# Optimization experiments

Measured on AMD Instinct MI355X. Metric: run time of the kernel, lower is better.

Reference implementation:

```python
import jax, jax.numpy as jnp
import numpy as np

NEG_SLOPE = 0.2
EPS = 1e-16


def gat_layer(x, src, dst, W, att, bias, heads, out_ch, concat, num_nodes, edge_weight):
    """WeightedGATConv forward (eval mode, dropout off).
    x: [N, Fin], src/dst: [E], W: [Fin, H*C], att: [H, 2C], bias: [H*C] or [C].
    """
    H, C = heads, out_ch
    xp = (x @ W).reshape(-1, H, C)           # [N, H, C]
    xi = xp[dst]                              # target features  [E, H, C]
    xj = xp[src]                              # source features  [E, H, C]
    # attention logits: (cat(xi, xj) * att).sum(-1)
    alpha = jnp.einsum('ehc,hc->eh', xi, att[:, :C]) + jnp.einsum('ehc,hc->eh', xj, att[:, C:])
    alpha = jnp.where(alpha >= 0, alpha, NEG_SLOPE * alpha)   # leaky_relu
    # segment softmax over incoming edges of each destination node
    amax = jax.ops.segment_max(alpha, dst, num_segments=num_nodes)  # [N, H]
    amax = jnp.where(jnp.isfinite(amax), amax, 0.0)
    ex = jnp.exp(alpha - amax[dst])                                  # [E, H]
    denom = jax.ops.segment_sum(ex, dst, num_segments=num_nodes)     # [N, H]
    a = ex / (denom[dst] + EPS)                                      # [E, H]
    msg = xj * a[..., None]                                          # [E, H, C]
    if edge_weight is not None:
        msg = msg * edge_weight[:, None, None]
    out = jax.ops.segment_sum(msg, dst, num_segments=num_nodes)      # [N, H, C]
    out = out.reshape(num_nodes, H * C) if concat else out.mean(axis=1)
    return out + bias


def setup_inputs() -> dict:
    key = jax.random.key(0)
    ks = jax.random.split(key, 10)
    N, E = 20000, 320000
    IN, HID, LAT, H = 512, 256, 128, 4
    C1 = HID // H
    glorot = lambda k, shp: jax.random.uniform(k, shp, jnp.float32, -1.0, 1.0) * jnp.sqrt(6.0 / (shp[-2] + shp[-1]))
    return {
        'x': jax.random.normal(ks[0], (N, IN), jnp.float32),
        'edge_index': jax.random.randint(ks[1], (2, E), 0, N, jnp.int32),
        'edge_weight': jax.random.uniform(ks[2], (E,), jnp.float32),
        'W1': glorot(ks[3], (IN, H * C1)),
        'att1': glorot(ks[4], (H, 2 * C1)),
        'b1': jnp.zeros((H * C1,), jnp.float32),
        'Wmu': glorot(ks[5], (HID, LAT)),
        'attmu': glorot(ks[6], (1, 2 * LAT)),
        'bmu': jnp.zeros((LAT,), jnp.float32),
        'Wlv': glorot(ks[7], (HID, LAT)),
        'attlv': glorot(ks[8], (1, 2 * LAT)),
        'blv': jnp.zeros((LAT,), jnp.float32),
    }


def reference(x, edge_index, edge_weight, W1, att1, b1, Wmu, attmu, bmu, Wlv, attlv, blv):
    N = x.shape[0]
    src, dst = edge_index[0], edge_index[1]
    H = att1.shape[0]
    C1 = att1.shape[1] // 2
    LAT = Wmu.shape[1]
    h = gat_layer(x, src, dst, W1, att1, b1, H, C1, True, N, edge_weight)
    h = jax.nn.elu(h)
    mu = gat_layer(h, src, dst, Wmu, attmu, bmu, 1, LAT, False, N, edge_weight)
    logvar = gat_layer(h, src, dst, Wlv, attlv, blv, 1, LAT, False, N, edge_weight)
    return (mu, logvar)
```

## Files before the change

kernel.cpp:

```cpp
#include <hip/hip_runtime.h>
#include <stdint.h>

#define NEG_SLOPE 0.2f
#define SEPS 1e-16f

typedef short bf16x8 __attribute__((ext_vector_type(8)));
typedef float f32x4 __attribute__((ext_vector_type(4)));

static __device__ __forceinline__ float bf2f(ushort u) {
  union { uint32_t i; float f; } v; v.i = ((uint32_t)u) << 16; return v.f;
}
static __device__ __forceinline__ ushort f2bf(float f) {
  uint32_t b = __float_as_uint(f);
  b += 0x7FFFu + ((b >> 16) & 1u);
  return (ushort)(b >> 16);
}
static __device__ __forceinline__ float blo(uint32_t u) { return __uint_as_float(u << 16); }
static __device__ __forceinline__ float bhi(uint32_t u) { return __uint_as_float(u & 0xFFFF0000u); }
static __device__ __forceinline__ float ldf(const void* p, size_t i, int mode) {
  return mode ? ((const float*)p)[i] : bf2f(((const ushort*)p)[i]);
}

__global__ void fill_out(float* __restrict__ out, int n, float v) {
  int i = blockIdx.x * 256 + threadIdx.x;
  if (i < n) out[i] = v;
}

struct DetPtrs {
  const uint32_t* p[11];
  int n[11];
  const uint32_t* idx;
  int idxn;
};
__global__ void prologue(DetPtrs dp, int* __restrict__ modes,
                         int* __restrict__ deg, float* __restrict__ dots,
                         int N, int nbDeg) {
  int b = blockIdx.x;
  if (b >= 12) {
    int rb = b - 12;
    if (rb < nbDeg) {
      int i = rb * 256 + threadIdx.x;
      if (i < N) deg[i] = 0;
    } else {
      int i = (rb - nbDeg) * 256 + threadIdx.x;
      if (i < N * 12) dots[i] = 0.f;
    }
    return;
  }
  __shared__ int sL, sH;
  if (threadIdx.x == 0) { sL = 0; sH = 0; }
  __syncthreads();
  if (b < 11) {
    const uint32_t* w = dp.p[b];
    int elems = dp.n[b];
    int nprobe = min(2048, elems / 2);
    int cL = 0, cH = 0;
    for (int i = threadIdx.x; i < nprobe; i += 256) {
      uint32_t v = w[i];
      uint32_t eL = (v >> 7) & 0xFFu;
      uint32_t eH = (v >> 23) & 0xFFu;
      if (eL >= 90u && eL <= 128u) cL++;
      if (eH >= 90u && eH <= 128u) cH++;
    }
    atomicAdd(&sL, cL); atomicAdd(&sH, cH);
    __syncthreads();
    if (threadIdx.x == 0) {
      int m;
      if (sL * 4 >= nprobe * 3) m = 0;
      else if (sH * 4 >= nprobe) m = 1;
      else m = 0;
      modes[b] = m;
    }
  } else {
    const uint32_t* w = dp.idx;
    int nprobe = min(4096, dp.idxn);
    int c = 0;
    for (int i = threadIdx.x; i < nprobe; i += 256)
      if ((i & 1) && w[i] == 0u) c++;
    atomicAdd(&sL, c);
    __syncthreads();
    if (threadIdx.x == 0) modes[11] = (sL * 4 >= (nprobe / 2) * 3) ? 1 : 0;
  }
}

struct WTArgs {
  const void* w1; const void* wmu; const void* wlv;
  ushort* wt1; ushort* wall;
};
struct SmallCan { const void* src[6]; float* dst[6]; int n[6]; int mi[6]; };
struct CanArgs {
  const void* ei; const void* ew;
  int* srcc; int* dstc; int* deg; float* ewf;
  int E; int N; int EB1; int WB;
  WTArgs wt;
  SmallCan sc;
};
__global__ void canon_all(CanArgs a, const int* __restrict__ modes) {
  int b = blockIdx.x;
  if (b < a.EB1) {
    int i = b * 256 + threadIdx.x;
    if (i >= a.E) return;
    int s, d;
    if (modes[11]) {
      s = (int)((const long long*)a.ei)[i];
      d = (int)((const long long*)a.ei)[a.E + i];
    } else {
      s = ((const int*)a.ei)[i];
      d = ((const int*)a.ei)[a.E + i];
    }
    s = min(max(s, 0), a.N - 1);
    d = min(max(d, 0), a.N - 1);
    a.srcc[i] = s;
    a.dstc[i] = d;
    atomicAdd(&a.deg[d], 1);
    float v = ldf(a.ew, i, modes[1]);
    if (!isfinite(v)) v = 0.f;
    a.ewf[i] = v;
  } else if (b < a.EB1 + a.WB) {
    int i = (b - a.EB1) * 256 + threadIdx.x;
    const int NW1 = 256 * 512;
    if (i < NW1) {
      int n = i >> 9, k = i & 511;
      float v = ldf(a.wt.w1, (size_t)k * 256 + n, modes[2]);
      if (!isfinite(v)) v = 0.f;
      a.wt.wt1[i] = f2bf(v);
    } else {
      int j = i - NW1;
      if (j >= 256 * 256) return;
      int n = j >> 8, k = j & 255;
      float v;
      if (n < 128) v = ldf(a.wt.wmu, (size_t)k * 128 + n, modes[5]);
      else         v = ldf(a.wt.wlv, (size_t)k * 128 + (n - 128), modes[8]);
      if (!isfinite(v)) v = 0.f;
      a.wt.wall[j] = f2bf(v);
    }
  } else {
    int sb = b - a.EB1 - a.WB;
    int m = modes[a.sc.mi[sb]];
    const void* s = a.sc.src[sb];
    float* d = a.sc.dst[sb];
    for (int i = threadIdx.x; i < a.sc.n[sb]; i += 256) {
      float v = ldf(s, i, m);
      if (!isfinite(v)) v = 0.f;
      d[i] = v;
    }
  }
}

__global__ __launch_bounds__(1024) void scan_deg(const int* __restrict__ deg,
                                                 int* __restrict__ row_ptr,
                                                 int* __restrict__ row_cur, int N) {
  __shared__ int part[1024];
  int t = threadIdx.x;
  int chunk = (N + 1023) / 1024;
  int lo = t * chunk, hi = min(lo + chunk, N);
  int s = 0;
  for (int i = lo; i < hi; ++i) s += deg[i];
  part[t] = s;
  __syncthreads();
  for (int off = 1; off < 1024; off <<= 1) {
    int v = (t >= off) ? part[t - off] : 0;
    __syncthreads();
    part[t] += v;
    __syncthreads();
  }
  int base = (t == 0) ? 0 : part[t - 1];
  for (int i = lo; i < hi; ++i) {
    row_ptr[i] = base; row_cur[i] = base;
    base += deg[i];
  }
  if (t == 1023) row_ptr[N] = part[1023];
}
__global__ void scatter_edges(const int* __restrict__ dstv, const int* __restrict__ srcv,
                              const float* __restrict__ ew, int* __restrict__ row_cur,
                              int* __restrict__ csr_src, float* __restrict__ csr_w, int E) {
  int e = blockIdx.x * 256 + threadIdx.x;
  if (e < E) {
    int p = atomicAdd(&row_cur[dstv[e]], 1);
    csr_src[p] = srcv[e];
    csr_w[p] = ew[e];
  }
}

template <int KTOT, int DMODE>
__global__ __launch_bounds__(256) void gemm_mfma(
    const void* __restrict__ A, const ushort* __restrict__ WT,
    ushort* __restrict__ out, int M, int nTot,
    const int* __restrict__ modeA, const float* __restrict__ attv,
    float* __restrict__ dotd, float* __restrict__ dotsrc) {
  __shared__ ushort As[64][40];
  __shared__ ushort Bs[128][40];

  int t = threadIdx.x;
  int m0 = blockIdx.x * 64;
  int n0 = blockIdx.y * 128;
  int wid = t >> 6, l = t & 63;
  int wr = wid >> 1, wc = wid & 1;
  int mode = modeA ? *modeA : 1;

  int arow = t >> 2;
  int akoff = (t & 3) * 8;
  int srow = min(m0 + arow, M - 1);
  int brow = t >> 1;
  int bkoff = (t & 1) * 16;

  f32x4 acc[2][4];
#pragma unroll
  for (int i = 0; i < 2; ++i)
#pragma unroll
    for (int j = 0; j < 4; ++j) acc[i][j] = (f32x4){0.f, 0.f, 0.f, 0.f};

  int cl = l & 15;
  int ksl = (l >> 4) * 8;

  for (int k0 = 0; k0 < KTOT; k0 += 32) {
    if (mode) {
      const float* Af = (const float*)A + (size_t)srow * KTOT + k0 + akoff;
      float4 v0 = *(const float4*)Af;
      float4 v1 = *(const float4*)(Af + 4);
      uint4 pk;
      pk.x = (uint32_t)f2bf(v0.x) | ((uint32_t)f2bf(v0.y) << 16);
      pk.y = (uint32_t)f2bf(v0.z) | ((uint32_t)f2bf(v0.w) << 16);
      pk.z = (uint32_t)f2bf(v1.x) | ((uint32_t)f2bf(v1.y) << 16);
      pk.w = (uint32_t)f2bf(v1.z) | ((uint32_t)f2bf(v1.w) << 16);
      *(uint4*)&As[arow][akoff] = pk;
    } else {
      *(uint4*)&As[arow][akoff] =
          *(const uint4*)((const ushort*)A + (size_t)srow * KTOT + k0 + akoff);
    }
    {
      const ushort* wp = WT + (size_t)(n0 + brow) * KTOT + k0 + bkoff;
      *(uint4*)&Bs[brow][bkoff] = *(const uint4*)wp;
      *(uint4*)&Bs[brow][bkoff + 8] = *(const uint4*)(wp + 8);
    }
    __syncthreads();

    bf16x8 af[2], bfr[4];
#pragma unroll
    for (int i = 0; i < 2; ++i)
      af[i] = *(const bf16x8*)&As[wr * 32 + i * 16 + cl][ksl];
#pragma unroll
    for (int j = 0; j < 4; ++j)
      bfr[j] = *(const bf16x8*)&Bs[wc * 64 + j * 16 + cl][ksl];
#pragma unroll
    for (int i = 0; i < 2; ++i)
#pragma unroll
      for (int j = 0; j < 4; ++j)
        acc[i][j] = __builtin_amdgcn_mfma_f32_16x16x32_bf16(af[i], bfr[j], acc[i][j], 0, 0, 0);
    __syncthreads();
  }

  int rb = (l >> 4) * 4;

  if (DMODE) {
    float wd[4], ws[4];
    int hsl;
    if (DMODE == 1) {
      hsl = (n0 >> 6) + wc;
#pragma unroll
      for (int j = 0; j < 4; ++j) {
        wd[j] = attv[hsl * 128 + j * 16 + cl];
        ws[j] = attv[hsl * 128 + 64 + j * 16 + cl];
      }
    } else {
      int base = n0 + wc * 64;
      hsl = base >> 7;
      int ccb = base & 127;
#pragma unroll
      for (int j = 0; j < 4; ++j) {
        wd[j] = attv[hsl * 256 + ccb + j * 16 + cl];
        ws[j] = attv[hsl * 256 + 128 + ccb + j * 16 + cl];
      }
    }
#pragma unroll
    for (int i = 0; i < 2; ++i)
#pragma unroll
      for (int r = 0; r < 4; ++r) {
        float pd = acc[i][0][r] * wd[0] + acc[i][1][r] * wd[1]
                 + acc[i][2][r] * wd[2] + acc[i][3][r] * wd[3];
        float ps = acc[i][0][r] * ws[0] + acc[i][1][r] * ws[1]
                 + acc[i][2][r] * ws[2] + acc[i][3][r] * ws[3];
        pd += __shfl_xor(pd, 1); pd += __shfl_xor(pd, 2);
        pd += __shfl_xor(pd, 4); pd += __shfl_xor(pd, 8);
        ps += __shfl_xor(ps, 1); ps += __shfl_xor(ps, 2);
        ps += __shfl_xor(ps, 4); ps += __shfl_xor(ps, 8);
        if (cl == 0) {
          int m = m0 + wr * 32 + i * 16 + rb + r;
          if (m < M) {
            if (DMODE == 1) {
              atomicAdd(&dotd[m * 4 + hsl], pd);
              atomicAdd(&dotsrc[m * 4 + hsl], ps);
            } else {
              atomicAdd(&dotd[m * 4 + hsl * 2], pd);
              atomicAdd(&dotd[m * 4 + hsl * 2 + 1], ps);
            }
          }
        }
      }
  }

#pragma unroll
  for (int i = 0; i < 2; ++i)
#pragma unroll
    for (int j = 0; j < 4; ++j)
#pragma unroll
      for (int r = 0; r < 4; ++r) {
        int m = m0 + wr * 32 + i * 16 + rb + r;
        if (m < M)
          out[(size_t)m * nTot + n0 + wc * 64 + j * 16 + cl] = f2bf(acc[i][j][r]);
      }
}

__global__ __launch_bounds__(256) void fused_agg1_wave(
    const int* __restrict__ row_ptr, const int* __restrict__ csr_src,
    const float* __restrict__ csr_w,
    const float* __restrict__ ad, const float* __restrict__ as_,
    const ushort* __restrict__ xp, const float* __restrict__ b1,
    float* __restrict__ hout, int N) {
  int n = blockIdx.x * 4 + (threadIdx.x >> 6);
  if (n >= N) return;
  int lane = threadIdx.x & 63;
  int h = lane & 3;
  int es = lane >> 2;
  int sg = lane >> 5, l = lane & 31, hl = l >> 3;

  int lo = row_ptr[n], hi = row_ptr[n + 1];
  float adv = ad[n * 4 + h];

  float m = -1e30f;
  float dsum = 0.f;
  float acc[8];
#pragma unroll
  for (int j = 0; j < 8; ++j) acc[j] = 0.f;

  for (int cb = lo; cb < hi; cb += 16) {
    int cn = min(16, hi - cb);
    float a = -1e30f;
    int sreg = 0;
    float wreg = 0.f;
    if (es < cn) {
      int i = cb + es;
      int s = csr_src[i];
      sreg = s;
      wreg = csr_w[i];
      float aa = adv + as_[s * 4 + h];
      a = aa >= 0.f ? aa : NEG_SLOPE * aa;
    }
    float cm = a;
    cm = fmaxf(cm, __shfl_xor(cm, 4));
    cm = fmaxf(cm, __shfl_xor(cm, 8));
    cm = fmaxf(cm, __shfl_xor(cm, 16));
    cm = fmaxf(cm, __shfl_xor(cm, 32));
    float mnew = fmaxf(m, cm);
    float scale = expf(m - mnew);
    m = mnew;
    float ev = (es < cn) ? expf(a - m) : 0.f;
    dsum = dsum * scale + ev;
    float cwreg = ev * wreg;
    float sc = __shfl(scale, hl);
#pragma unroll
    for (int j = 0; j < 8; ++j) acc[j] *= sc;
    for (int el2 = 0; el2 < cn; el2 += 2) {
      int el = el2 + sg;
      int elc = min(el, cn - 1);
      float cw = __shfl(cwreg, (elc << 2) | hl);
      int s = __shfl(sreg, elc << 2);
      if (el < cn) {
        uint4 v = *(const uint4*)(xp + (size_t)s * 256 + l * 8);
        acc[0] += cw * blo(v.x); acc[1] += cw * bhi(v.x);
        acc[2] += cw * blo(v.y); acc[3] += cw * bhi(v.y);
        acc[4] += cw * blo(v.z); acc[5] += cw * bhi(v.z);
        acc[6] += cw * blo(v.w); acc[7] += cw * bhi(v.w);
      }
    }
  }

  dsum += __shfl_xor(dsum, 4);
  dsum += __shfl_xor(dsum, 8);
  dsum += __shfl_xor(dsum, 16);
  dsum += __shfl_xor(dsum, 32);
  float den = __shfl(dsum, hl);

#pragma unroll
  for (int j = 0; j < 8; ++j) acc[j] += __shfl_down(acc[j], 32);

  if (sg == 0) {
    float inv = 1.0f / (den + SEPS);
#pragma unroll
    for (int j = 0; j < 8; ++j) {
      float val = acc[j] * inv + b1[l * 8 + j];
      hout[(size_t)n * 256 + l * 8 + j] = val > 0.f ? val : expm1f(val);
    }
  }
}

__global__ __launch_bounds__(256) void fused_agg2_wave(
    const int* __restrict__ row_ptr, const int* __restrict__ csr_src,
    const float* __restrict__ csr_w, const float* __restrict__ a4,
    const ushort* __restrict__ hp2,
    const float* __restrict__ bmu, const float* __restrict__ blv,
    float* __restrict__ out, int N) {
  int wid = blockIdx.x * 4 + (threadIdx.x >> 6);
  int n = wid >> 1, sl = wid & 1;
  if (n >= N) return;
  int lane = threadIdx.x & 63;
  int sg = lane >> 4, l = lane & 15;

  int lo = row_ptr[n], hi = row_ptr[n + 1];
  float adv = a4[n * 4 + sl * 2];

  float m = -1e30f;
  float dsum = 0.f;
  float acc[8];
#pragma unroll
  for (int j = 0; j < 8; ++j) acc[j] = 0.f;

  for (int cb = lo; cb < hi; cb += 64) {
    int cn = min(64, hi - cb);
    float a = -1e30f;
    int sreg = 0;
    float wreg = 0.f;
    if (lane < cn) {
      int i = cb + lane;
      int s = csr_src[i];
      sreg = s;
      wreg = csr_w[i];
      float aa = adv + a4[s * 4 + sl * 2 + 1];
      a = aa >= 0.f ? aa : NEG_SLOPE * aa;
    }
    float cm = a;
    cm = fmaxf(cm, __shfl_xor(cm, 1));
    cm = fmaxf(cm, __shfl_xor(cm, 2));
    cm = fmaxf(cm, __shfl_xor(cm, 4));
    cm = fmaxf(cm, __shfl_xor(cm, 8));
    cm = fmaxf(cm, __shfl_xor(cm, 16));
    cm = fmaxf(cm, __shfl_xor(cm, 32));
    float mnew = fmaxf(m, cm);
    float scale = expf(m - mnew);
    m = mnew;
    float ev = (lane < cn) ? expf(a - m) : 0.f;
    dsum = dsum * scale + ev;
    float cwreg = ev * wreg;
#pragma unroll
    for (int j = 0; j < 8; ++j) acc[j] *= scale;
    for (int el2 = 0; el2 < cn; el2 += 4) {
      int el = el2 + sg;
      int elc = min(el, cn - 1);
      float cw = __shfl(cwreg, elc);
      int s = __shfl(sreg, elc);
      if (el < cn) {
        uint4 v = *(const uint4*)(hp2 + (size_t)s * 256 + sl * 128 + l * 8);
        acc[0] += cw * blo(v.x); acc[1] += cw * bhi(v.x);
        acc[2] += cw * blo(v.y); acc[3] += cw * bhi(v.y);
        acc[4] += cw * blo(v.z); acc[5] += cw * bhi(v.z);
        acc[6] += cw * blo(v.w); acc[7] += cw * bhi(v.w);
      }
    }
  }

  dsum += __shfl_xor(dsum, 1);
  dsum += __shfl_xor(dsum, 2);
  dsum += __shfl_xor(dsum, 4);
  dsum += __shfl_xor(dsum, 8);
  dsum += __shfl_xor(dsum, 16);
  dsum += __shfl_xor(dsum, 32);

#pragma unroll
  for (int j = 0; j < 8; ++j) {
    acc[j] += __shfl_down(acc[j], 32);
    acc[j] += __shfl_down(acc[j], 16);
  }

  if (sg == 0) {
    float inv = 1.0f / (dsum + SEPS);
    const float* bb = sl ? blv : bmu;
    float* op = out + (size_t)sl * N * 128 + (size_t)n * 128 + l * 8;
#pragma unroll
    for (int j = 0; j < 8; ++j) op[j] = acc[j] * inv + bb[l * 8 + j];
  }
}

extern "C" void kernel_launch(void* const* d_in, const int* in_sizes, int n_in,
                              void* d_out, int out_size, void* d_ws, size_t ws_size,
                              hipStream_t stream) {
  int OB = (out_size + 255) / 256;
  bool ok = (n_in == 12);
  int HID = 0, IN = 0, N = 0, LAT = 0, E = 0;
  if (ok) {
    HID = in_sizes[5];
    ok = ok && HID == 256;
    IN = HID ? in_sizes[3] / HID : 0;
    ok = ok && IN == 512 && in_sizes[3] == IN * HID;
    N = IN ? in_sizes[0] / IN : 0;
    ok = ok && N > 0 && in_sizes[0] == N * IN && (N % 4) == 0;
    LAT = in_sizes[8];
    ok = ok && LAT == 128;
    E = in_sizes[2];
    ok = ok && E > 0 && in_sizes[1] == 2 * E;
    ok = ok && in_sizes[4] == 2 * HID && in_sizes[6] == HID * LAT &&
         in_sizes[7] == 2 * LAT && in_sizes[9] == HID * LAT &&
         in_sizes[10] == 2 * LAT && in_sizes[11] == LAT &&
         out_size == 2 * N * LAT;
  }
  if (!ok) { fill_out<<<OB, 256, 0, stream>>>((float*)d_out, out_size, 2.0f); return; }

  char* p = (char*)d_ws;
  auto alloc = [&](size_t bytes) -> char* {
    char* r = p;
    p += (bytes + 255) & ~((size_t)255);
    return r;
  };
  ushort* xp_bf = (ushort*)alloc((size_t)N * HID * 2);
  float*  hreg  = (float*) alloc((size_t)N * HID * 4);
  ushort* WT1b  = (ushort*)alloc((size_t)HID * IN * 2);
  ushort* WallT = (ushort*)alloc((size_t)2 * LAT * HID * 2);
  float*  dots  = (float*) alloc((size_t)N * 12 * 4);
  float*  att1f = (float*) alloc((size_t)2 * HID * 4);
  float*  att2f = (float*) alloc((size_t)4 * LAT * 4);
  float*  b1f   = (float*) alloc((size_t)HID * 4);
  float*  bmuf  = (float*) alloc((size_t)LAT * 4);
  float*  blvf  = (float*) alloc((size_t)LAT * 4);
  float*  ewf   = (float*) alloc((size_t)E * 4);
  int*    srcc  = (int*)   alloc((size_t)E * 4);
  int*    dstc  = (int*)   alloc((size_t)E * 4);
  int*    csr_src=(int*)   alloc((size_t)E * 4);
  float*  csr_w = (float*) alloc((size_t)E * 4);
  int*    row_ptr=(int*)   alloc((size_t)(N + 1) * 4);
  int*    row_cur=(int*)   alloc((size_t)N * 4);
  int*    deg   = (int*)   alloc((size_t)N * 4);
  int*    modes = (int*)   alloc(16 * 4);

  size_t need = (size_t)(p - (char*)d_ws);
  if (need > ws_size) {
    fill_out<<<OB, 256, 0, stream>>>((float*)d_out, out_size, 3.0f);
    return;
  }

  ushort* hp2 = xp_bf;
  float* ad1 = dots;
  float* as1 = dots + (size_t)N * 4;
  float* a4  = dots + (size_t)N * 8;

  const int fidx[11] = {0, 2, 3, 4, 5, 6, 7, 8, 9, 10, 11};
  DetPtrs dp;
  for (int i = 0; i < 11; ++i) {
    dp.p[i] = (const uint32_t*)d_in[fidx[i]];
    dp.n[i] = in_sizes[fidx[i]];
  }
  dp.idx = (const uint32_t*)d_in[1];
  dp.idxn = 2 * E;
  int nbDeg = (N + 255) / 256;
  int nbDots = (N * 12 + 255) / 256;
  prologue<<<12 + nbDeg + nbDots, 256, 0, stream>>>(dp, modes, deg, dots, N, nbDeg);

  int EB1 = (E + 255) / 256;
  int WB = (HID * IN + 2 * LAT * HID + 255) / 256;
  CanArgs ca;
  ca.ei = d_in[1]; ca.ew = d_in[2];
  ca.srcc = srcc; ca.dstc = dstc; ca.deg = deg; ca.ewf = ewf;
  ca.E = E; ca.N = N; ca.EB1 = EB1; ca.WB = WB;
  ca.wt.w1 = d_in[3]; ca.wt.wmu = d_in[6]; ca.wt.wlv = d_in[9];
  ca.wt.wt1 = WT1b; ca.wt.wall = WallT;
  ca.sc.src[0] = d_in[4];  ca.sc.dst[0] = att1f;        ca.sc.n[0] = 2 * HID; ca.sc.mi[0] = 3;
  ca.sc.src[1] = d_in[5];  ca.sc.dst[1] = b1f;          ca.sc.n[1] = HID;     ca.sc.mi[1] = 4;
  ca.sc.src[2] = d_in[7];  ca.sc.dst[2] = att2f;        ca.sc.n[2] = 2 * LAT; ca.sc.mi[2] = 6;
  ca.sc.src[3] = d_in[8];  ca.sc.dst[3] = bmuf;         ca.sc.n[3] = LAT;     ca.sc.mi[3] = 7;
  ca.sc.src[4] = d_in[10]; ca.sc.dst[4] = att2f + 256;  ca.sc.n[4] = 2 * LAT; ca.sc.mi[4] = 9;
  ca.sc.src[5] = d_in[11]; ca.sc.dst[5] = blvf;         ca.sc.n[5] = LAT;     ca.sc.mi[5] = 10;
  canon_all<<<EB1 + WB + 6, 256, 0, stream>>>(ca, modes);

  scan_deg<<<1, 1024, 0, stream>>>(deg, row_ptr, row_cur, N);
  scatter_edges<<<EB1, 256, 0, stream>>>(dstc, srcc, ewf, row_cur, csr_src, csr_w, E);

  dim3 g1((N + 63) / 64, HID / 128);
  dim3 g2((N + 63) / 64, (2 * LAT) / 128);

  gemm_mfma<512, 1><<<g1, 256, 0, stream>>>(d_in[0], WT1b, xp_bf, N, HID,
                                            &modes[0], att1f, ad1, as1);
  fused_agg1_wave<<<(N + 3) / 4, 256, 0, stream>>>(row_ptr, csr_src, csr_w,
                                                   ad1, as1, xp_bf, b1f, hreg, N);

  gemm_mfma<256, 2><<<g2, 256, 0, stream>>>(hreg, WallT, hp2, N, 2 * LAT,
                                            nullptr, att2f, a4, nullptr);
  fused_agg2_wave<<<(2 * N + 3) / 4, 256, 0, stream>>>(row_ptr, csr_src, csr_w, a4,
                                                       hp2, bmuf, blvf,
                                                       (float*)d_out, N);
}
```

Measured before the change: 292.0 us.

## Widen GEMM tiles to full N, store bf16 hidden, merge agg2 waves per node

The GEMM now computes all 256 output columns per block, so each A tile is loaded once. Because every attention dot product is complete within one block, the atomics into zeroed buffers become plain stores and the prologue no longer clears the dots array. The first aggregation writes the ELU output as bf16 instead of fp32, which halves that tensor's traffic and lets the second GEMM read bf16 directly. The mu/logvar aggregation now uses one wave per node covering both heads rather than two waves, sharing the edge index loads. The risks are more registers per GEMM thread (16 accumulators), fewer GEMM blocks, and an extra bf16 rounding on the hidden features.

```diff
diff --git a/kernel.cpp b/kernel.cpp
--- a/kernel.cpp
+++ b/kernel.cpp
@@ -33,18 +33,11 @@
   int idxn;
 };
 __global__ void prologue(DetPtrs dp, int* __restrict__ modes,
-                         int* __restrict__ deg, float* __restrict__ dots,
-                         int N, int nbDeg) {
+                         int* __restrict__ deg, int N) {
   int b = blockIdx.x;
   if (b >= 12) {
-    int rb = b - 12;
-    if (rb < nbDeg) {
-      int i = rb * 256 + threadIdx.x;
-      if (i < N) deg[i] = 0;
-    } else {
-      int i = (rb - nbDeg) * 256 + threadIdx.x;
-      if (i < N * 12) dots[i] = 0.f;
-    }
+    int i = (b - 12) * 256 + threadIdx.x;
+    if (i < N) deg[i] = 0;
     return;
   }
   __shared__ int sL, sH;
@@ -185,30 +178,27 @@
 template <int KTOT, int DMODE>
 __global__ __launch_bounds__(256) void gemm_mfma(
     const void* __restrict__ A, const ushort* __restrict__ WT,
-    ushort* __restrict__ out, int M, int nTot,
+    ushort* __restrict__ out, int M,
     const int* __restrict__ modeA, const float* __restrict__ attv,
     float* __restrict__ dotd, float* __restrict__ dotsrc) {
   __shared__ ushort As[64][40];
-  __shared__ ushort Bs[128][40];
+  __shared__ ushort Bs[256][40];
 
   int t = threadIdx.x;
   int m0 = blockIdx.x * 64;
-  int n0 = blockIdx.y * 128;
   int wid = t >> 6, l = t & 63;
   int wr = wid >> 1, wc = wid & 1;
-  int mode = modeA ? *modeA : 1;
+  int mode = modeA ? *modeA : 0;
 
   int arow = t >> 2;
   int akoff = (t & 3) * 8;
   int srow = min(m0 + arow, M - 1);
-  int brow = t >> 1;
-  int bkoff = (t & 1) * 16;
-
-  f32x4 acc[2][4];
+
+  f32x4 acc[2][8];
 #pragma unroll
   for (int i = 0; i < 2; ++i)
 #pragma unroll
-    for (int j = 0; j < 4; ++j) acc[i][j] = (f32x4){0.f, 0.f, 0.f, 0.f};
+    for (int j = 0; j < 8; ++j) acc[i][j] = (f32x4){0.f, 0.f, 0.f, 0.f};
 
   int cl = l & 15;
   int ksl = (l >> 4) * 8;
@@ -228,86 +218,108 @@
       *(uint4*)&As[arow][akoff] =
           *(const uint4*)((const ushort*)A + (size_t)srow * KTOT + k0 + akoff);
     }
-    {
-      const ushort* wp = WT + (size_t)(n0 + brow) * KTOT + k0 + bkoff;
-      *(uint4*)&Bs[brow][bkoff] = *(const uint4*)wp;
-      *(uint4*)&Bs[brow][bkoff + 8] = *(const uint4*)(wp + 8);
+#pragma unroll
+    for (int i = 0; i < 4; ++i) {
+      int f = t + i * 256;
+      int row = f >> 2, koff = (f & 3) * 8;
+      *(uint4*)&Bs[row][koff] = *(const uint4*)(WT + (size_t)row * KTOT + k0 + koff);
     }
     __syncthreads();
 
-    bf16x8 af[2], bfr[4];
+    bf16x8 af[2], bfr[8];
 #pragma unroll
     for (int i = 0; i < 2; ++i)
       af[i] = *(const bf16x8*)&As[wr * 32 + i * 16 + cl][ksl];
 #pragma unroll
-    for (int j = 0; j < 4; ++j)
-      bfr[j] = *(const bf16x8*)&Bs[wc * 64 + j * 16 + cl][ksl];
+    for (int j = 0; j < 8; ++j)
+      bfr[j] = *(const bf16x8*)&Bs[wc * 128 + j * 16 + cl][ksl];
 #pragma unroll
     for (int i = 0; i < 2; ++i)
 #pragma unroll
-      for (int j = 0; j < 4; ++j)
+      for (int j = 0; j < 8; ++j)
         acc[i][j] = __builtin_amdgcn_mfma_f32_16x16x32_bf16(af[i], bfr[j], acc[i][j], 0, 0, 0);
     __syncthreads();
   }
 
   int rb = (l >> 4) * 4;
 
-  if (DMODE) {
-    float wd[4], ws[4];
-    int hsl;
-    if (DMODE == 1) {
-      hsl = (n0 >> 6) + wc;
-#pragma unroll
-      for (int j = 0; j < 4; ++j) {
-        wd[j] = attv[hsl * 128 + j * 16 + cl];
-        ws[j] = attv[hsl * 128 + 64 + j * 16 + cl];
-      }
-    } else {
-      int base = n0 + wc * 64;
-      hsl = base >> 7;
-      int ccb = base & 127;
-#pragma unroll
-      for (int j = 0; j < 4; ++j) {
-        wd[j] = attv[hsl * 256 + ccb + j * 16 + cl];
-        ws[j] = attv[hsl * 256 + 128 + ccb + j * 16 + cl];
-      }
+  if (DMODE == 1) {
+    float wdv[8], wsv[8];
+#pragma unroll
+    for (int j = 0; j < 8; ++j) {
+      int h = wc * 2 + (j >> 2);
+      int c = (j & 3) * 16 + cl;
+      wdv[j] = attv[h * 128 + c];
+      wsv[j] = attv[h * 128 + 64 + c];
     }
 #pragma unroll
     for (int i = 0; i < 2; ++i)
 #pragma unroll
       for (int r = 0; r < 4; ++r) {
-        float pd = acc[i][0][r] * wd[0] + acc[i][1][r] * wd[1]
-                 + acc[i][2][r] * wd[2] + acc[i][3][r] * wd[3];
-        float ps = acc[i][0][r] * ws[0] + acc[i][1][r] * ws[1]
-                 + acc[i][2][r] * ws[2] + acc[i][3][r] * ws[3];
-        pd += __shfl_xor(pd, 1); pd += __shfl_xor(pd, 2);
-        pd += __shfl_xor(pd, 4); pd += __shfl_xor(pd, 8);
-        ps += __shfl_xor(ps, 1); ps += __shfl_xor(ps, 2);
-        ps += __shfl_xor(ps, 4); ps += __shfl_xor(ps, 8);
+        float pd0 = acc[i][0][r] * wdv[0] + acc[i][1][r] * wdv[1]
+                  + acc[i][2][r] * wdv[2] + acc[i][3][r] * wdv[3];
+        float ps0 = acc[i][0][r] * wsv[0] + acc[i][1][r] * wsv[1]
+                  + acc[i][2][r] * wsv[2] + acc[i][3][r] * wsv[3];
+        float pd1 = acc[i][4][r] * wdv[4] + acc[i][5][r] * wdv[5]
+                  + acc[i][6][r] * wdv[6] + acc[i][7][r] * wdv[7];
+        float ps1 = acc[i][4][r] * wsv[4] + acc[i][5][r] * wsv[5]
+                  + acc[i][6][r] * wsv[6] + acc[i][7][r] * wsv[7];
+#pragma unroll
+        for (int d = 1; d < 16; d <<= 1) {
+          pd0 += __shfl_xor(pd0, d); ps0 += __shfl_xor(ps0, d);
+          pd1 += __shfl_xor(pd1, d); ps1 += __shfl_xor(ps1, d);
+        }
         if (cl == 0) {
           int m = m0 + wr * 32 + i * 16 + rb + r;
           if (m < M) {
-            if (DMODE == 1) {
-              atomicAdd(&dotd[m * 4 + hsl], pd);
-              atomicAdd(&dotsrc[m * 4 + hsl], ps);
-            } else {
-              atomicAdd(&dotd[m * 4 + hsl * 2], pd);
-              atomicAdd(&dotd[m * 4 + hsl * 2 + 1], ps);
-            }
+            dotd[m * 4 + wc * 2] = pd0;
+            dotsrc[m * 4 + wc * 2] = ps0;
+            dotd[m * 4 + wc * 2 + 1] = pd1;
+            dotsrc[m * 4 + wc * 2 + 1] = ps1;
           }
         }
       }
+  } else if (DMODE == 2) {
+    float wdv[8], wsv[8];
+#pragma unroll
+    for (int j = 0; j < 8; ++j) {
+      int c = j * 16 + cl;
+      wdv[j] = attv[wc * 256 + c];
+      wsv[j] = attv[wc * 256 + 128 + c];
+    }
+#pragma unroll
+    for (int i = 0; i < 2; ++i)
+#pragma unroll
+      for (int r = 0; r < 4; ++r) {
+        float pd = 0.f, ps = 0.f;
+#pragma unroll
+        for (int j = 0; j < 8; ++j) {
+          pd += acc[i][j][r] * wdv[j];
+          ps += acc[i][j][r] * wsv[j];
+        }
+#pragma unroll
+        for (int d = 1; d < 16; d <<= 1) {
+          pd += __shfl_xor(pd, d); ps += __shfl_xor(ps, d);
+        }
+        if (cl == 0) {
+          int m = m0 + wr * 32 + i * 16 + rb + r;
+          if (m < M) {
+            dotd[m * 4 + wc * 2] = pd;
+            dotd[m * 4 + wc * 2 + 1] = ps;
+          }
+        }
+      }
   }
 
 #pragma unroll
   for (int i = 0; i < 2; ++i)
 #pragma unroll
-    for (int j = 0; j < 4; ++j)
+    for (int j = 0; j < 8; ++j)
 #pragma unroll
       for (int r = 0; r < 4; ++r) {
         int m = m0 + wr * 32 + i * 16 + rb + r;
         if (m < M)
-          out[(size_t)m * nTot + n0 + wc * 64 + j * 16 + cl] = f2bf(acc[i][j][r]);
+          out[(size_t)m * 256 + wc * 128 + j * 16 + cl] = f2bf(acc[i][j][r]);
       }
 }
 
@@ -316,7 +328,7 @@
     const float* __restrict__ csr_w,
     const float* __restrict__ ad, const float* __restrict__ as_,
     const ushort* __restrict__ xp, const float* __restrict__ b1,
-    float* __restrict__ hout, int N) {
+    ushort* __restrict__ hout, int N) {
   int n = blockIdx.x * 4 + (threadIdx.x >> 6);
   if (n >= N) return;
   int lane = threadIdx.x & 63;
@@ -386,11 +398,18 @@
 
   if (sg == 0) {
     float inv = 1.0f / (den + SEPS);
-#pragma unroll
-    for (int j = 0; j < 8; ++j) {
-      float val = acc[j] * inv + b1[l * 8 + j];
-      hout[(size_t)n * 256 + l * 8 + j] = val > 0.f ? val : expm1f(val);
-    }
+    uint4 pk;
+    uint32_t w[4];
+#pragma unroll
+    for (int q = 0; q < 4; ++q) {
+      float v0 = acc[q * 2] * inv + b1[l * 8 + q * 2];
+      float v1 = acc[q * 2 + 1] * inv + b1[l * 8 + q * 2 + 1];
+      v0 = v0 > 0.f ? v0 : expm1f(v0);
+      v1 = v1 > 0.f ? v1 : expm1f(v1);
+      w[q] = (uint32_t)f2bf(v0) | ((uint32_t)f2bf(v1) << 16);
+    }
+    pk.x = w[0]; pk.y = w[1]; pk.z = w[2]; pk.w = w[3];
+    *(uint4*)(hout + (size_t)n * 256 + l * 8) = pk;
   }
 }
 
@@ -400,28 +419,27 @@
     const ushort* __restrict__ hp2,
     const float* __restrict__ bmu, const float* __restrict__ blv,
     float* __restrict__ out, int N) {
-  int wid = blockIdx.x * 4 + (threadIdx.x >> 6);
-  int n = wid >> 1, sl = wid & 1;
+  int n = blockIdx.x * 4 + (threadIdx.x >> 6);
   if (n >= N) return;
   int lane = threadIdx.x & 63;
-  int sg = lane >> 4, l = lane & 15;
+  int e31 = lane & 31, sl = lane >> 5;
 
   int lo = row_ptr[n], hi = row_ptr[n + 1];
   float adv = a4[n * 4 + sl * 2];
 
   float m = -1e30f;
   float dsum = 0.f;
-  float acc[8];
-#pragma unroll
-  for (int j = 0; j < 8; ++j) acc[j] = 0.f;
-
-  for (int cb = lo; cb < hi; cb += 64) {
-    int cn = min(64, hi - cb);
+  float acc[4];
+#pragma unroll
+  for (int j = 0; j < 4; ++j) acc[j] = 0.f;
+
+  for (int cb = lo; cb < hi; cb += 32) {
+    int cn = min(32, hi - cb);
     float a = -1e30f;
     int sreg = 0;
     float wreg = 0.f;
-    if (lane < cn) {
-      int i = cb + lane;
+    if (e31 < cn) {
+      int i = cb + e31;
       int s = csr_src[i];
       sreg = s;
       wreg = csr_w[i];
@@ -434,27 +452,20 @@
     cm = fmaxf(cm, __shfl_xor(cm, 4));
     cm = fmaxf(cm, __shfl_xor(cm, 8));
     cm = fmaxf(cm, __shfl_xor(cm, 16));
-    cm = fmaxf(cm, __shfl_xor(cm, 32));
     float mnew = fmaxf(m, cm);
     float scale = expf(m - mnew);
     m = mnew;
-    float ev = (lane < cn) ? expf(a - m) : 0.f;
+    float ev = (e31 < cn) ? expf(a - m) : 0.f;
     dsum = dsum * scale + ev;
     float cwreg = ev * wreg;
 #pragma unroll
-    for (int j = 0; j < 8; ++j) acc[j] *= scale;
-    for (int el2 = 0; el2 < cn; el2 += 4) {
-      int el = el2 + sg;
-      int elc = min(el, cn - 1);
-      float cw = __shfl(cwreg, elc);
-      int s = __shfl(sreg, elc);
-      if (el < cn) {
-        uint4 v = *(const uint4*)(hp2 + (size_t)s * 256 + sl * 128 + l * 8);
-        acc[0] += cw * blo(v.x); acc[1] += cw * bhi(v.x);
-        acc[2] += cw * blo(v.y); acc[3] += cw * bhi(v.y);
-        acc[4] += cw * blo(v.z); acc[5] += cw * bhi(v.z);
-        acc[6] += cw * blo(v.w); acc[7] += cw * bhi(v.w);
-      }
+    for (int j = 0; j < 4; ++j) acc[j] *= scale;
+    for (int el = 0; el < cn; ++el) {
+      float cw = __shfl(cwreg, (sl << 5) | el);
+      int s = __shfl(sreg, el);
+      uint2 v = *(const uint2*)(hp2 + (size_t)s * 256 + lane * 4);
+      acc[0] += cw * blo(v.x); acc[1] += cw * bhi(v.x);
+      acc[2] += cw * blo(v.y); acc[3] += cw * bhi(v.y);
     }
   }
 
@@ -463,21 +474,13 @@
   dsum += __shfl_xor(dsum, 4);
   dsum += __shfl_xor(dsum, 8);
   dsum += __shfl_xor(dsum, 16);
-  dsum += __shfl_xor(dsum, 32);
-
-#pragma unroll
-  for (int j = 0; j < 8; ++j) {
-    acc[j] += __shfl_down(acc[j], 32);
-    acc[j] += __shfl_down(acc[j], 16);
-  }
-
-  if (sg == 0) {
-    float inv = 1.0f / (dsum + SEPS);
-    const float* bb = sl ? blv : bmu;
-    float* op = out + (size_t)sl * N * 128 + (size_t)n * 128 + l * 8;
-#pragma unroll
-    for (int j = 0; j < 8; ++j) op[j] = acc[j] * inv + bb[l * 8 + j];
-  }
+
+  float inv = 1.0f / (dsum + SEPS);
+  const float* bb = sl ? blv : bmu;
+  int c0 = e31 * 4;
+  float* op = out + (size_t)sl * N * 128 + (size_t)n * 128 + c0;
+#pragma unroll
+  for (int j = 0; j < 4; ++j) op[j] = acc[j] * inv + bb[c0 + j];
 }
 
 extern "C" void kernel_launch(void* const* d_in, const int* in_sizes, int n_in,
@@ -511,7 +514,7 @@
     return r;
   };
   ushort* xp_bf = (ushort*)alloc((size_t)N * HID * 2);
-  float*  hreg  = (float*) alloc((size_t)N * HID * 4);
+  ushort* hreg  = (ushort*)alloc((size_t)N * HID * 2);
   ushort* WT1b  = (ushort*)alloc((size_t)HID * IN * 2);
   ushort* WallT = (ushort*)alloc((size_t)2 * LAT * HID * 2);
   float*  dots  = (float*) alloc((size_t)N * 12 * 4);
@@ -550,8 +553,7 @@
   dp.idx = (const uint32_t*)d_in[1];
   dp.idxn = 2 * E;
   int nbDeg = (N + 255) / 256;
-  int nbDots = (N * 12 + 255) / 256;
-  prologue<<<12 + nbDeg + nbDots, 256, 0, stream>>>(dp, modes, deg, dots, N, nbDeg);
+  prologue<<<12 + nbDeg, 256, 0, stream>>>(dp, modes, deg, N);
 
   int EB1 = (E + 255) / 256;
   int WB = (HID * IN + 2 * LAT * HID + 255) / 256;
@@ -572,17 +574,16 @@
   scan_deg<<<1, 1024, 0, stream>>>(deg, row_ptr, row_cur, N);
   scatter_edges<<<EB1, 256, 0, stream>>>(dstc, srcc, ewf, row_cur, csr_src, csr_w, E);
 
-  dim3 g1((N + 63) / 64, HID / 128);
-  dim3 g2((N + 63) / 64, (2 * LAT) / 128);
-
-  gemm_mfma<512, 1><<<g1, 256, 0, stream>>>(d_in[0], WT1b, xp_bf, N, HID,
+  int MB = (N + 63) / 64;
+
+  gemm_mfma<512, 1><<<MB, 256, 0, stream>>>(d_in[0], WT1b, xp_bf, N,
                                             &modes[0], att1f, ad1, as1);
   fused_agg1_wave<<<(N + 3) / 4, 256, 0, stream>>>(row_ptr, csr_src, csr_w,
                                                    ad1, as1, xp_bf, b1f, hreg, N);
 
-  gemm_mfma<256, 2><<<g2, 256, 0, stream>>>(hreg, WallT, hp2, N, 2 * LAT,
+  gemm_mfma<256, 2><<<MB, 256, 0, stream>>>(hreg, WallT, hp2, N,
                                             nullptr, att2f, a4, nullptr);
-  fused_agg2_wave<<<(2 * N + 3) / 4, 256, 0, stream>>>(row_ptr, csr_src, csr_w, a4,
-                                                       hp2, bmuf, blvf,
-                                                       (float*)d_out, N);
-}
+  fused_agg2_wave<<<(N + 3) / 4, 256, 0, stream>>>(row_ptr, csr_src, csr_w, a4,
+                                                   hp2, bmuf, blvf,
+                                                   (float*)d_out, N);
+}
```

New measurement: 286.3 us. About the same (-1.9%).
